# Kernel tuning notes

Hardware: AMD Instinct MI355X
Metric: run time of the kernel (lower is better)

The kernel has to match this reference:

```python
import jax, jax.numpy as jnp
import numpy as np

EPS = 1e-6

def _normalize(v):
    return v / jnp.sqrt(jnp.maximum(jnp.sum(v * v, -1, keepdims=True), EPS))

def _frames(pos):
    # backbone rigid frame from N (atom 0), CA (atom 1), C (atom 2) via Gram-Schmidt
    n, ca, c = pos[..., 0, :], pos[..., 1, :], pos[..., 2, :]
    e1 = _normalize(c - ca)
    v2 = n - ca
    e2 = _normalize(v2 - jnp.sum(e1 * v2, -1, keepdims=True) * e1)
    e3 = jnp.cross(e1, e2)
    R = jnp.stack([e1, e2, e3], axis=-1)  # columns are the local basis
    return R, ca

def _vnorm(d):
    return jnp.sqrt(jnp.maximum(jnp.sum(d * d, -1), EPS))

def setup_inputs():
    L, N, A = 2, 768, 14
    key = jax.random.key(0)
    k1, k2, k3, k4, k5 = jax.random.split(key, 5)
    pred = 3.0 * jax.random.normal(k1, (L, N, A, 3), dtype=jnp.float32)
    gt = 3.0 * jax.random.normal(k2, (N, A, 3), dtype=jnp.float32)
    atom_mask = (jax.random.uniform(k3, (N, A)) > 0.1).astype(jnp.float32)
    batch = jnp.sort(jax.random.randint(k4, (N,), 0, 2)).astype(jnp.int32)
    chain = jnp.sort(jax.random.randint(k5, (N,), 0, 4)).astype(jnp.int32)
    return {"pred": pred, "gt": gt, "atom_mask": atom_mask, "batch": batch, "chain": chain}

def reference(pred, gt, atom_mask, batch, chain):
    L, N, A, _ = pred.shape
    same_item = (batch[:, None] == batch[None, :]).astype(pred.dtype)
    # pair_mask[i, j, a] = mask[i, a] * mask[j, a] * same_item[i, j]
    pair_mask = atom_mask[:, None] * atom_mask[None, :] * same_item[..., None]
    Rp, tp = _frames(pred)   # [L,N,3,3], [L,N,3]
    Rg, tg = _frames(gt)     # [N,3,3],   [N,3]
    # pglobal[l,i,j,a] = Rp[l,i]^T @ (pred[l,j,a] - tp[l,i]) (frame-inverse point application)
    pglobal = (jnp.einsum('lidk,ljad->lijak', Rp, pred)
               - jnp.einsum('lidk,lid->lik', Rp, tp)[:, :, None, None, :])
    gglobal = (jnp.einsum('idk,jad->ijak', Rg, gt)
               - jnp.einsum('idk,id->ik', Rg, tg)[:, None, None, :])
    err = _vnorm(pglobal - gglobal[None])                       # [L,N,N,A]
    fape = jnp.where(pair_mask[None] > 0, err, 0.0).sum(-1)
    fape = fape / jnp.maximum(pair_mask[None].sum(-1), 1e-6)    # [L,N,N]
    rotamer_error = jnp.diagonal(fape, 0, -2, -1)               # [L,N]
    res_mask = (atom_mask > 0).any(-1)
    n_res = jnp.maximum(res_mask.astype(pred.dtype).sum(), 1e-6)
    rotamer_loss = rotamer_error.sum(-1) / n_res                # [L]
    pm2 = (pair_mask > 0).any(-1).astype(pred.dtype)            # [N,N]
    final_ae = fape[-1]
    same_chain = (chain[:, None] == chain[None, :]).astype(pred.dtype) * pm2
    other_chain = (chain[:, None] != chain[None, :]).astype(pred.dtype) * pm2
    # intra/inter coins in the source are zeros_like(bernoulli) == always False -> clip at 10
    clipped = jnp.clip(fape, 0.0, 10.0)
    intra = (clipped * same_chain[None]).sum((-1, -2))
    intra = intra / jnp.maximum(same_chain.sum(), 1e-6) / 10.0
    inter = (clipped * other_chain[None]).sum((-1, -2))
    inter = inter / jnp.maximum(other_chain.sum(), 1e-6) / 10.0
    fape_loss = intra + inter                                   # [L]
    # lDDT on CA atoms (atom index 1) for the last prediction step
    gt_ca = gt[:, 1, :]
    pred_ca = pred[-1, :, 1, :]
    gt_d = _vnorm(gt_ca[:, None] - gt_ca[None, :])
    rm = res_mask.astype(jnp.float32)
    dmask = ((gt_d < 15.0).astype(jnp.float32) * rm[:, None] * rm[None, :]
             * (1.0 - jnp.eye(N, dtype=jnp.float32))).astype(bool)
    d = _vnorm(pred_ca[:, None] - pred_ca[None, :])
    derr = jnp.where(dmask, jnp.abs(gt_d - d), jnp.inf)
    thresholds = jnp.array([0.5, 1.0, 2.0, 4.0], dtype=jnp.float32)
    l = (derr[..., None] < thresholds).astype(jnp.float32).mean(-1)
    lddt_val = jnp.where(dmask, l, 0.0).sum(-1)
    lddt_val = lddt_val / jnp.maximum(dmask.astype(jnp.float32).sum(-1), 1e-6)
    return (fape_loss, rotamer_loss, final_ae, rotamer_error[-1], lddt_val)
```

## Files before the change

### kernel.cpp

```cpp
#include <hip/hip_runtime.h>
#include <math.h>

#define EPS 1e-6f
#define IPB 3

struct F3 { float x, y, z; };
__device__ inline F3 sub3(F3 a, F3 b){return {a.x-b.x,a.y-b.y,a.z-b.z};}
__device__ inline float dot3(F3 a, F3 b){return a.x*b.x+a.y*b.y+a.z*b.z;}
__device__ inline F3 scale3(F3 a,float s){return {a.x*s,a.y*s,a.z*s};}
__device__ inline F3 cross3(F3 a,F3 b){return {a.y*b.z-a.z*b.y, a.z*b.x-a.x*b.z, a.x*b.y-a.y*b.x};}
__device__ inline F3 norm3(F3 v){float s=dot3(v,v);float inv=1.f/sqrtf(fmaxf(s,EPS));return scale3(v,inv);}

__device__ inline void make_frame(const float* __restrict__ base, float R[9], F3& ca) {
    F3 n = {base[0], base[1], base[2]};
    ca   = {base[3], base[4], base[5]};
    F3 c = {base[6], base[7], base[8]};
    F3 e1 = norm3(sub3(c, ca));
    F3 v2 = sub3(n, ca);
    float d = dot3(e1, v2);
    F3 e2 = norm3({v2.x - d*e1.x, v2.y - d*e1.y, v2.z - d*e1.z});
    F3 e3 = cross3(e1, e2);
    R[0]=e1.x; R[1]=e1.y; R[2]=e1.z;
    R[3]=e2.x; R[4]=e2.y; R[5]=e2.z;
    R[6]=e3.x; R[7]=e3.y; R[8]=e3.z;
}

__global__ __launch_bounds__(256) void prep_all_kernel(
    const float* __restrict__ pred, const float* __restrict__ gt,
    const float* __restrict__ atom_mask, const int* __restrict__ batch,
    const int* __restrict__ chain,
    float* __restrict__ Mc, int* __restrict__ packed,
    float* __restrict__ gtca, float* __restrict__ predca,
    float4* __restrict__ predT4, float4* __restrict__ gtT4,
    int L, int N, int A)
{
    int idx = blockIdx.x * blockDim.x + threadIdx.x;

    int totalT = (L + 1) * A * N;
    if (idx < totalT) {
        int z = idx / (A * N);
        int r = idx - z * (A * N);
        int a = r / N;
        int j = r - a * N;
        if (z < L) {
            const float* s = pred + (((size_t)z * N + j) * A + a) * 3;
            predT4[((size_t)z * A + a) * N + j] = make_float4(s[0], s[1], s[2], 0.f);
        } else {
            const float* s = gt + ((size_t)j * A + a) * 3;
            gtT4[(size_t)a * N + j] = make_float4(s[0], s[1], s[2], 0.f);
        }
    }

    if (idx >= L * N) return;
    int l = idx / N, i = idx - l * N;

    float Rg[9]; F3 cag;
    make_frame(gt + (size_t)i * A * 3, Rg, cag);
    float Rp[9]; F3 cap;
    make_frame(pred + ((size_t)l * N + i) * A * 3, Rp, cap);

    float m[9];
    #pragma unroll
    for (int d = 0; d < 3; d++)
        #pragma unroll
        for (int e = 0; e < 3; e++)
            m[d*3+e] = Rp[0*3+d]*Rg[0*3+e] + Rp[1*3+d]*Rg[1*3+e] + Rp[2*3+d]*Rg[2*3+e];
    float c0 = cap.x - (m[0]*cag.x + m[1]*cag.y + m[2]*cag.z);
    float c1 = cap.y - (m[3]*cag.x + m[4]*cag.y + m[5]*cag.z);
    float c2 = cap.z - (m[6]*cag.x + m[7]*cag.y + m[8]*cag.z);

    float* o = Mc + (size_t)idx * 12;
    #pragma unroll
    for (int k = 0; k < 9; k++) o[k] = m[k];
    o[9] = c0; o[10] = c1; o[11] = c2;

    if (l == 0) {
        unsigned mm = 0;
        for (int a = 0; a < A; a++)
            if (atom_mask[(size_t)i * A + a] > 0.f) mm |= (1u << a);
        packed[i] = (int)(mm | ((unsigned)batch[i] << 16) | ((unsigned)chain[i] << 24));
        gtca[i*3] = cag.x; gtca[i*3+1] = cag.y; gtca[i*3+2] = cag.z;
    }
    if (l == L - 1) { predca[i*3] = cap.x; predca[i*3+1] = cap.y; predca[i*3+2] = cap.z; }
}

__global__ __launch_bounds__(256) void fape_kernel(
    const float4* __restrict__ predT4, const float4* __restrict__ gtT4,
    const float* __restrict__ Mc, const int* __restrict__ packed,
    const float* __restrict__ gtca, const float* __restrict__ predca,
    float* __restrict__ part,
    float* __restrict__ out_final, float* __restrict__ out_rot,
    float* __restrict__ out_lddt,
    int L, int N)
{
    int t = threadIdx.x;
    int ib = blockIdx.x, l = blockIdx.y;
    int i0 = ib * IPB;
    bool last = (l == L - 1);

    const float* __restrict__ mcp = Mc + ((size_t)l * N + i0) * 12;
    float M[IPB][12];
    #pragma unroll
    for (int q = 0; q < IPB; q++)
        #pragma unroll
        for (int k = 0; k < 12; k++) M[q][k] = mcp[q*12 + k];

    int mk[IPB], bt[IPB], ch[IPB];
    #pragma unroll
    for (int q = 0; q < IPB; q++) {
        int pk = packed[i0 + q];
        mk[q] = pk & 0xFFFF; bt[q] = (pk >> 16) & 0xFF; ch[q] = (pk >> 24) & 0xFF;
    }

    float gx[IPB],gy[IPB],gz[IPB],px[IPB],py[IPB],pz[IPB];
    #pragma unroll
    for (int q = 0; q < IPB; q++) { gx[q]=gy[q]=gz[q]=px[q]=py[q]=pz[q]=0.f; }
    if (last) {
        #pragma unroll
        for (int q = 0; q < IPB; q++) {
            int i = i0 + q;
            gx[q]=gtca[i*3]; gy[q]=gtca[i*3+1]; gz[q]=gtca[i*3+2];
            px[q]=predca[i*3]; py[q]=predca[i*3+1]; pz[q]=predca[i*3+2];
        }
    }

    const float4* __restrict__ xT4 = predT4 + (size_t)l * 14 * N;

    float a_ss=0.f, a_so=0.f, a_cs=0.f, a_co=0.f, a_rot=0.f;
    float ls[IPB], lc[IPB];
    #pragma unroll
    for (int q = 0; q < IPB; q++) { ls[q]=0.f; lc[q]=0.f; }

    for (int j = t; j < N; j += 256) {
        int pkj = packed[j];
        int mskj = pkj & 0xFFFF;
        int bj = (pkj >> 16) & 0xFF, cj = (pkj >> 24) & 0xFF;

        int mj[IPB]; bool pm[IPB]; bool anyp = false;
        #pragma unroll
        for (int q = 0; q < IPB; q++) {
            mj[q] = mk[q] & mskj;
            pm[q] = (bj == bt[q]) && (mj[q] != 0);
            anyp = anyp || pm[q];
        }
        float num[IPB];
        #pragma unroll
        for (int q = 0; q < IPB; q++) num[q] = 0.f;

        if (__any((int)anyp)) {
            #pragma unroll
            for (int a = 0; a < 14; a++) {
                float4 Y = gtT4[(size_t)a * N + j];
                float4 X = xT4[(size_t)a * N + j];
                #pragma unroll
                for (int q = 0; q < IPB; q++) {
                    float d0 = X.x - (M[q][0]*Y.x + M[q][1]*Y.y + M[q][2]*Y.z + M[q][9]);
                    float d1 = X.y - (M[q][3]*Y.x + M[q][4]*Y.y + M[q][5]*Y.z + M[q][10]);
                    float d2 = X.z - (M[q][6]*Y.x + M[q][7]*Y.y + M[q][8]*Y.z + M[q][11]);
                    num[q] += (float)((mj[q] >> a) & 1) * sqrtf(fmaxf(d0*d0+d1*d1+d2*d2, EPS));
                }
            }
        }

        #pragma unroll
        for (int q = 0; q < IPB; q++) {
            float fv = pm[q] ? num[q] / (float)__popc((unsigned)mj[q]) : 0.f;
            int i = i0 + q;
            if (last) {
                out_final[(size_t)i * N + j] = fv;
                if (j == i) out_rot[i] = fv;
            }
            if (j == i) a_rot += fv;
            if (pm[q]) {
                float cl = fminf(fv, 10.f);
                if (ch[q] == cj) { a_ss += cl; a_cs += 1.f; } else { a_so += cl; a_co += 1.f; }
            }
        }

        if (last) {
            float4 CG = gtT4[(size_t)N + j];
            float4 CP = xT4[(size_t)N + j];
            #pragma unroll
            for (int q = 0; q < IPB; q++) {
                if ((mk[q] != 0) && (mskj != 0) && (j != i0 + q)) {
                    float dx=gx[q]-CG.x, dy=gy[q]-CG.y, dz=gz[q]-CG.z;
                    float gd = sqrtf(fmaxf(dx*dx+dy*dy+dz*dz, EPS));
                    if (gd < 15.f) {
                        float ex=px[q]-CP.x, ey=py[q]-CP.y, ez=pz[q]-CP.z;
                        float pd = sqrtf(fmaxf(ex*ex+ey*ey+ez*ez, EPS));
                        float de = fabsf(gd - pd);
                        ls[q] += ((de<0.5f?1.f:0.f)+(de<1.f?1.f:0.f)+(de<2.f?1.f:0.f)+(de<4.f?1.f:0.f))*0.25f;
                        lc[q] += 1.f;
                    }
                }
            }
        }
    }

    float vals[11];
    vals[0]=a_ss; vals[1]=a_so; vals[2]=a_cs; vals[3]=a_co; vals[4]=a_rot;
    #pragma unroll
    for (int q = 0; q < IPB; q++) { vals[5+q]=ls[q]; vals[5+IPB+q]=lc[q]; }
    #pragma unroll
    for (int k = 0; k < 11; k++)
        for (int o = 32; o > 0; o >>= 1) vals[k] += __shfl_down(vals[k], o, 64);

    __shared__ float red[4][11];
    int wave = t >> 6, lane = t & 63;
    if (lane == 0) {
        #pragma unroll
        for (int k = 0; k < 11; k++) red[wave][k] = vals[k];
    }
    __syncthreads();
    if (t == 0) {
        float v[11];
        #pragma unroll
        for (int k = 0; k < 11; k++)
            v[k] = red[0][k] + red[1][k] + red[2][k] + red[3][k];
        float* p = part + ((size_t)l * (N / IPB) + ib) * 8;
        p[0]=v[0]; p[1]=v[1]; p[2]=v[2]; p[3]=v[3]; p[4]=v[4];
        if (last) {
            #pragma unroll
            for (int q = 0; q < IPB; q++)
                out_lddt[i0 + q] = v[5+q] / fmaxf(v[5+IPB+q], 1e-6f);
        }
    }
}

__global__ __launch_bounds__(256) void reduce_kernel(
    const int* __restrict__ packed, const float* __restrict__ part,
    float* __restrict__ out, int L, int N)
{
    int t = threadIdx.x;
    int BPL = N / IPB;
    float ss[4]={0,0,0,0}, so[4]={0,0,0,0}, rt[4]={0,0,0,0};
    float cs=0.f, co=0.f;
    for (int b = t; b < BPL * L; b += 256) {
        int l = b / BPL;
        const float* p = part + (size_t)b * 8;
        ss[l] += p[0]; so[l] += p[1]; rt[l] += p[4];
        if (l == 0) { cs += p[2]; co += p[3]; }
    }
    float nr = 0.f;
    for (int i = t; i < N; i += 256)
        nr += ((packed[i] & 0xFFFF) != 0) ? 1.f : 0.f;

    __shared__ float red[4];
    int wave = t >> 6, lane = t & 63;
    float vals[11];
    vals[0]=cs; vals[1]=co; vals[2]=nr;
    for (int l = 0; l < L; l++) { vals[3+l]=ss[l]; vals[3+L+l]=so[l]; vals[3+2*L+l]=rt[l]; }
    float res[11];
    for (int k = 0; k < 3 + 3*L; k++) {
        float v = vals[k];
        for (int o = 32; o > 0; o >>= 1) v += __shfl_down(v, o, 64);
        __syncthreads();
        if (lane == 0) red[wave] = v;
        __syncthreads();
        res[k] = red[0] + red[1] + red[2] + red[3];
    }
    if (t == 0) {
        float csf = fmaxf(res[0], 1e-6f);
        float cof = fmaxf(res[1], 1e-6f);
        float nrm = fmaxf(res[2], 1e-6f);
        for (int l = 0; l < L; l++) {
            out[l]     = res[3+l] / csf / 10.f + res[3+L+l] / cof / 10.f;
            out[L + l] = res[3+2*L+l] / nrm;
        }
    }
}

extern "C" void kernel_launch(void* const* d_in, const int* in_sizes, int n_in,
                              void* d_out, int out_size, void* d_ws, size_t ws_size,
                              hipStream_t stream)
{
    const float* pred      = (const float*)d_in[0];
    const float* gt        = (const float*)d_in[1];
    const float* atom_mask = (const float*)d_in[2];
    const int*   batch     = (const int*)d_in[3];
    const int*   chain     = (const int*)d_in[4];

    int N = in_sizes[3];
    int A = in_sizes[2] / N;
    int L = in_sizes[0] / (N * A * 3);

    float* out = (float*)d_out;
    float* out_final = out + 2 * L;
    float* out_rot   = out_final + (size_t)N * N;
    float* out_lddt  = out_rot + N;

    float* ws = (float*)d_ws;
    float4* predT4 = (float4*)ws;
    float4* gtT4   = predT4 + (size_t)L * A * N;
    float*  Mc     = (float*)(gtT4 + (size_t)A * N);
    float*  gtca   = Mc + (size_t)L * N * 12;
    float*  predca = gtca + (size_t)N * 3;
    float*  part   = predca + (size_t)N * 3;
    int*    packed = (int*)(part + (size_t)L * (N / IPB) * 8);

    int totalT = (L + 1) * A * N;
    prep_all_kernel<<<(totalT + 255) / 256, 256, 0, stream>>>(
        pred, gt, atom_mask, batch, chain,
        Mc, packed, gtca, predca, predT4, gtT4, L, N, A);

    dim3 grid(N / IPB, L);
    fape_kernel<<<grid, 256, 0, stream>>>(
        predT4, gtT4, Mc, packed, gtca, predca, part,
        out_final, out_rot, out_lddt, L, N);

    reduce_kernel<<<1, 256, 0, stream>>>(packed, part, out, L, N);
}
```

Measured before the change: 96.68 us.

## Split FAPE j-range across blocks and shrink rows per block

The FAPE kernel's j loop is split into three slices across extra grid blocks, and rows per block drop from 3 to 2. This raises the block count so the many CUs get more parallel work, with each thread handling one j. Per-slice partials, including the lDDT sums, are written to a larger partial buffer. The final lDDT division moves into the single-block reduce kernel. The cost is more redundant per-block frame loads and more reduction work done serially in one block.

```diff
diff --git a/kernel.cpp b/kernel.cpp
--- a/kernel.cpp
+++ b/kernel.cpp
@@ -2,7 +2,8 @@
 #include <math.h>
 
 #define EPS 1e-6f
-#define IPB 3
+#define IPB 2
+#define JS  3
 
 struct F3 { float x, y, z; };
 __device__ inline F3 sub3(F3 a, F3 b){return {a.x-b.x,a.y-b.y,a.z-b.z};}
@@ -90,12 +91,14 @@
     const float* __restrict__ gtca, const float* __restrict__ predca,
     float* __restrict__ part,
     float* __restrict__ out_final, float* __restrict__ out_rot,
-    float* __restrict__ out_lddt,
     int L, int N)
 {
     int t = threadIdx.x;
-    int ib = blockIdx.x, l = blockIdx.y;
+    int ib = blockIdx.x;
+    int l  = blockIdx.y / JS;
+    int s  = blockIdx.y - l * JS;
     int i0 = ib * IPB;
+    int jlo = s * (N / JS), jhi = jlo + (N / JS);
     bool last = (l == L - 1);
 
     const float* __restrict__ mcp = Mc + ((size_t)l * N + i0) * 12;
@@ -131,7 +134,7 @@
     #pragma unroll
     for (int q = 0; q < IPB; q++) { ls[q]=0.f; lc[q]=0.f; }
 
-    for (int j = t; j < N; j += 256) {
+    for (int j = jlo + t; j < jhi; j += 256) {
         int pkj = packed[j];
         int mskj = pkj & 0xFFFF;
         int bj = (pkj >> 16) & 0xFF, cj = (pkj >> 24) & 0xFF;
@@ -197,60 +200,68 @@
         }
     }
 
-    float vals[11];
+    float vals[9];
     vals[0]=a_ss; vals[1]=a_so; vals[2]=a_cs; vals[3]=a_co; vals[4]=a_rot;
     #pragma unroll
     for (int q = 0; q < IPB; q++) { vals[5+q]=ls[q]; vals[5+IPB+q]=lc[q]; }
     #pragma unroll
-    for (int k = 0; k < 11; k++)
+    for (int k = 0; k < 9; k++)
         for (int o = 32; o > 0; o >>= 1) vals[k] += __shfl_down(vals[k], o, 64);
 
-    __shared__ float red[4][11];
+    __shared__ float red[4][9];
     int wave = t >> 6, lane = t & 63;
     if (lane == 0) {
         #pragma unroll
-        for (int k = 0; k < 11; k++) red[wave][k] = vals[k];
+        for (int k = 0; k < 9; k++) red[wave][k] = vals[k];
     }
     __syncthreads();
     if (t == 0) {
-        float v[11];
-        #pragma unroll
-        for (int k = 0; k < 11; k++)
-            v[k] = red[0][k] + red[1][k] + red[2][k] + red[3][k];
-        float* p = part + ((size_t)l * (N / IPB) + ib) * 8;
-        p[0]=v[0]; p[1]=v[1]; p[2]=v[2]; p[3]=v[3]; p[4]=v[4];
-        if (last) {
-            #pragma unroll
-            for (int q = 0; q < IPB; q++)
-                out_lddt[i0 + q] = v[5+q] / fmaxf(v[5+IPB+q], 1e-6f);
-        }
+        float* p = part + ((size_t)blockIdx.y * (N / IPB) + ib) * 12;
+        #pragma unroll
+        for (int k = 0; k < 9; k++)
+            p[k] = red[0][k] + red[1][k] + red[2][k] + red[3][k];
     }
 }
 
 __global__ __launch_bounds__(256) void reduce_kernel(
     const int* __restrict__ packed, const float* __restrict__ part,
-    float* __restrict__ out, int L, int N)
+    float* __restrict__ out, float* __restrict__ out_lddt, int L, int N)
 {
     int t = threadIdx.x;
     int BPL = N / IPB;
+    int ROWS = L * JS;
+
     float ss[4]={0,0,0,0}, so[4]={0,0,0,0}, rt[4]={0,0,0,0};
     float cs=0.f, co=0.f;
-    for (int b = t; b < BPL * L; b += 256) {
-        int l = b / BPL;
-        const float* p = part + (size_t)b * 8;
+    for (int b = t; b < ROWS * BPL; b += 256) {
+        int row = b / BPL;
+        int l = row / JS;
+        const float* p = part + (size_t)b * 12;
         ss[l] += p[0]; so[l] += p[1]; rt[l] += p[4];
         if (l == 0) { cs += p[2]; co += p[3]; }
     }
+
+    for (int i = t; i < N; i += 256) {
+        int ib = i / IPB, q = i - ib * IPB;
+        float lsum = 0.f, lcnt = 0.f;
+        for (int s = 0; s < JS; s++) {
+            const float* p = part + (((size_t)((L - 1) * JS + s)) * BPL + ib) * 12;
+            lsum += p[5 + q];
+            lcnt += p[5 + IPB + q];
+        }
+        out_lddt[i] = lsum / fmaxf(lcnt, 1e-6f);
+    }
+
     float nr = 0.f;
     for (int i = t; i < N; i += 256)
         nr += ((packed[i] & 0xFFFF) != 0) ? 1.f : 0.f;
 
     __shared__ float red[4];
     int wave = t >> 6, lane = t & 63;
-    float vals[11];
+    float vals[15];
     vals[0]=cs; vals[1]=co; vals[2]=nr;
     for (int l = 0; l < L; l++) { vals[3+l]=ss[l]; vals[3+L+l]=so[l]; vals[3+2*L+l]=rt[l]; }
-    float res[11];
+    float res[15];
     for (int k = 0; k < 3 + 3*L; k++) {
         float v = vals[k];
         for (int o = 32; o > 0; o >>= 1) v += __shfl_down(v, o, 64);
@@ -296,17 +307,17 @@
     float*  gtca   = Mc + (size_t)L * N * 12;
     float*  predca = gtca + (size_t)N * 3;
     float*  part   = predca + (size_t)N * 3;
-    int*    packed = (int*)(part + (size_t)L * (N / IPB) * 8);
+    int*    packed = (int*)(part + (size_t)L * JS * (N / IPB) * 12);
 
     int totalT = (L + 1) * A * N;
     prep_all_kernel<<<(totalT + 255) / 256, 256, 0, stream>>>(
         pred, gt, atom_mask, batch, chain,
         Mc, packed, gtca, predca, predT4, gtT4, L, N, A);
 
-    dim3 grid(N / IPB, L);
+    dim3 grid(N / IPB, L * JS);
     fape_kernel<<<grid, 256, 0, stream>>>(
         predT4, gtT4, Mc, packed, gtca, predca, part,
-        out_final, out_rot, out_lddt, L, N);
-
-    reduce_kernel<<<1, 256, 0, stream>>>(packed, part, out, L, N);
-}
+        out_final, out_rot, L, N);
+
+    reduce_kernel<<<1, 256, 0, stream>>>(packed, part, out, out_lddt, L, N);
+}
```

Result: faster. 93.11 us (-3.7%).

## Fuse prep into FAPE kernel, read raw AoS inputs, and use two residues per block

Applied to the files above, without the earlier changes.

Removes the separate prep kernel that transposed coordinates into float4 SoA buffers and precomputed frames. Each FAPE block now builds its own frame-composition matrices and atom-mask bits directly from the raw inputs, and reads per-j coordinates as contiguous 42-float rows into registers. IPB drops from 3 to 2, so there are more blocks. This saves one launch and the workspace round trip. In exchange, every block recomputes the mask bits for all j, and the strided AoS loads coalesce worse than the old SoA float4 loads.

```diff
diff --git a/kernel.cpp b/kernel.cpp
--- a/kernel.cpp
+++ b/kernel.cpp
@@ -2,7 +2,9 @@
 #include <math.h>
 
 #define EPS 1e-6f
-#define IPB 3
+#define IPB 2
+#define NA 14
+#define ROW 42
 
 struct F3 { float x, y, z; };
 __device__ inline F3 sub3(F3 a, F3 b){return {a.x-b.x,a.y-b.y,a.z-b.z};}
@@ -25,69 +27,10 @@
     R[6]=e3.x; R[7]=e3.y; R[8]=e3.z;
 }
 
-__global__ __launch_bounds__(256) void prep_all_kernel(
+__global__ __launch_bounds__(256) void fape_kernel(
     const float* __restrict__ pred, const float* __restrict__ gt,
     const float* __restrict__ atom_mask, const int* __restrict__ batch,
     const int* __restrict__ chain,
-    float* __restrict__ Mc, int* __restrict__ packed,
-    float* __restrict__ gtca, float* __restrict__ predca,
-    float4* __restrict__ predT4, float4* __restrict__ gtT4,
-    int L, int N, int A)
-{
-    int idx = blockIdx.x * blockDim.x + threadIdx.x;
-
-    int totalT = (L + 1) * A * N;
-    if (idx < totalT) {
-        int z = idx / (A * N);
-        int r = idx - z * (A * N);
-        int a = r / N;
-        int j = r - a * N;
-        if (z < L) {
-            const float* s = pred + (((size_t)z * N + j) * A + a) * 3;
-            predT4[((size_t)z * A + a) * N + j] = make_float4(s[0], s[1], s[2], 0.f);
-        } else {
-            const float* s = gt + ((size_t)j * A + a) * 3;
-            gtT4[(size_t)a * N + j] = make_float4(s[0], s[1], s[2], 0.f);
-        }
-    }
-
-    if (idx >= L * N) return;
-    int l = idx / N, i = idx - l * N;
-
-    float Rg[9]; F3 cag;
-    make_frame(gt + (size_t)i * A * 3, Rg, cag);
-    float Rp[9]; F3 cap;
-    make_frame(pred + ((size_t)l * N + i) * A * 3, Rp, cap);
-
-    float m[9];
-    #pragma unroll
-    for (int d = 0; d < 3; d++)
-        #pragma unroll
-        for (int e = 0; e < 3; e++)
-            m[d*3+e] = Rp[0*3+d]*Rg[0*3+e] + Rp[1*3+d]*Rg[1*3+e] + Rp[2*3+d]*Rg[2*3+e];
-    float c0 = cap.x - (m[0]*cag.x + m[1]*cag.y + m[2]*cag.z);
-    float c1 = cap.y - (m[3]*cag.x + m[4]*cag.y + m[5]*cag.z);
-    float c2 = cap.z - (m[6]*cag.x + m[7]*cag.y + m[8]*cag.z);
-
-    float* o = Mc + (size_t)idx * 12;
-    #pragma unroll
-    for (int k = 0; k < 9; k++) o[k] = m[k];
-    o[9] = c0; o[10] = c1; o[11] = c2;
-
-    if (l == 0) {
-        unsigned mm = 0;
-        for (int a = 0; a < A; a++)
-            if (atom_mask[(size_t)i * A + a] > 0.f) mm |= (1u << a);
-        packed[i] = (int)(mm | ((unsigned)batch[i] << 16) | ((unsigned)chain[i] << 24));
-        gtca[i*3] = cag.x; gtca[i*3+1] = cag.y; gtca[i*3+2] = cag.z;
-    }
-    if (l == L - 1) { predca[i*3] = cap.x; predca[i*3+1] = cap.y; predca[i*3+2] = cap.z; }
-}
-
-__global__ __launch_bounds__(256) void fape_kernel(
-    const float4* __restrict__ predT4, const float4* __restrict__ gtT4,
-    const float* __restrict__ Mc, const int* __restrict__ packed,
-    const float* __restrict__ gtca, const float* __restrict__ predca,
     float* __restrict__ part,
     float* __restrict__ out_final, float* __restrict__ out_rot,
     float* __restrict__ out_lddt,
@@ -98,33 +41,36 @@
     int i0 = ib * IPB;
     bool last = (l == L - 1);
 
-    const float* __restrict__ mcp = Mc + ((size_t)l * N + i0) * 12;
     float M[IPB][12];
-    #pragma unroll
-    for (int q = 0; q < IPB; q++)
-        #pragma unroll
-        for (int k = 0; k < 12; k++) M[q][k] = mcp[q*12 + k];
-
     int mk[IPB], bt[IPB], ch[IPB];
+    float gx[IPB],gy[IPB],gz[IPB],px[IPB],py[IPB],pz[IPB];
     #pragma unroll
     for (int q = 0; q < IPB; q++) {
-        int pk = packed[i0 + q];
-        mk[q] = pk & 0xFFFF; bt[q] = (pk >> 16) & 0xFF; ch[q] = (pk >> 24) & 0xFF;
-    }
-
-    float gx[IPB],gy[IPB],gz[IPB],px[IPB],py[IPB],pz[IPB];
-    #pragma unroll
-    for (int q = 0; q < IPB; q++) { gx[q]=gy[q]=gz[q]=px[q]=py[q]=pz[q]=0.f; }
-    if (last) {
-        #pragma unroll
-        for (int q = 0; q < IPB; q++) {
-            int i = i0 + q;
-            gx[q]=gtca[i*3]; gy[q]=gtca[i*3+1]; gz[q]=gtca[i*3+2];
-            px[q]=predca[i*3]; py[q]=predca[i*3+1]; pz[q]=predca[i*3+2];
-        }
-    }
-
-    const float4* __restrict__ xT4 = predT4 + (size_t)l * 14 * N;
+        int i = i0 + q;
+        float Rg[9]; F3 cag;
+        make_frame(gt + (size_t)i * ROW, Rg, cag);
+        float Rp[9]; F3 cap;
+        make_frame(pred + ((size_t)l * N + i) * ROW, Rp, cap);
+        #pragma unroll
+        for (int d = 0; d < 3; d++)
+            #pragma unroll
+            for (int e = 0; e < 3; e++)
+                M[q][d*3+e] = Rp[0*3+d]*Rg[0*3+e] + Rp[1*3+d]*Rg[1*3+e] + Rp[2*3+d]*Rg[2*3+e];
+        M[q][9]  = cap.x - (M[q][0]*cag.x + M[q][1]*cag.y + M[q][2]*cag.z);
+        M[q][10] = cap.y - (M[q][3]*cag.x + M[q][4]*cag.y + M[q][5]*cag.z);
+        M[q][11] = cap.z - (M[q][6]*cag.x + M[q][7]*cag.y + M[q][8]*cag.z);
+
+        unsigned mm = 0;
+        const float* am = atom_mask + (size_t)i * NA;
+        #pragma unroll
+        for (int a = 0; a < NA; a++) mm |= (am[a] > 0.f) ? (1u << a) : 0u;
+        mk[q] = (int)mm; bt[q] = batch[i]; ch[q] = chain[i];
+
+        gx[q]=cag.x; gy[q]=cag.y; gz[q]=cag.z;
+        px[q]=cap.x; py[q]=cap.y; pz[q]=cap.z;
+    }
+
+    const float* __restrict__ Xbase = pred + (size_t)l * N * ROW;
 
     float a_ss=0.f, a_so=0.f, a_cs=0.f, a_co=0.f, a_rot=0.f;
     float ls[IPB], lc[IPB];
@@ -132,14 +78,19 @@
     for (int q = 0; q < IPB; q++) { ls[q]=0.f; lc[q]=0.f; }
 
     for (int j = t; j < N; j += 256) {
-        int pkj = packed[j];
-        int mskj = pkj & 0xFFFF;
-        int bj = (pkj >> 16) & 0xFF, cj = (pkj >> 24) & 0xFF;
+        unsigned mskj = 0;
+        const float* amj = atom_mask + (size_t)j * NA;
+        #pragma unroll
+        for (int a = 0; a < NA; a++) mskj |= (amj[a] > 0.f) ? (1u << a) : 0u;
+        int bj = batch[j], cj = chain[j];
+
+        const float* __restrict__ Yp = gt + (size_t)j * ROW;
+        const float* __restrict__ Xp = Xbase + (size_t)j * ROW;
 
         int mj[IPB]; bool pm[IPB]; bool anyp = false;
         #pragma unroll
         for (int q = 0; q < IPB; q++) {
-            mj[q] = mk[q] & mskj;
+            mj[q] = mk[q] & (int)mskj;
             pm[q] = (bj == bt[q]) && (mj[q] != 0);
             anyp = anyp || pm[q];
         }
@@ -149,15 +100,22 @@
 
         if (__any((int)anyp)) {
             #pragma unroll
-            for (int a = 0; a < 14; a++) {
-                float4 Y = gtT4[(size_t)a * N + j];
-                float4 X = xT4[(size_t)a * N + j];
+            for (int ah = 0; ah < 2; ah++) {
+                float xr[21], yr[21];
                 #pragma unroll
-                for (int q = 0; q < IPB; q++) {
-                    float d0 = X.x - (M[q][0]*Y.x + M[q][1]*Y.y + M[q][2]*Y.z + M[q][9]);
-                    float d1 = X.y - (M[q][3]*Y.x + M[q][4]*Y.y + M[q][5]*Y.z + M[q][10]);
-                    float d2 = X.z - (M[q][6]*Y.x + M[q][7]*Y.y + M[q][8]*Y.z + M[q][11]);
-                    num[q] += (float)((mj[q] >> a) & 1) * sqrtf(fmaxf(d0*d0+d1*d1+d2*d2, EPS));
+                for (int k = 0; k < 21; k++) { xr[k] = Xp[ah*21 + k]; yr[k] = Yp[ah*21 + k]; }
+                #pragma unroll
+                for (int a = 0; a < 7; a++) {
+                    int aa = ah*7 + a;
+                    float Yx = yr[a*3], Yy = yr[a*3+1], Yz = yr[a*3+2];
+                    float Xx = xr[a*3], Xy = xr[a*3+1], Xz = xr[a*3+2];
+                    #pragma unroll
+                    for (int q = 0; q < IPB; q++) {
+                        float d0 = Xx - (M[q][0]*Yx + M[q][1]*Yy + M[q][2]*Yz + M[q][9]);
+                        float d1 = Xy - (M[q][3]*Yx + M[q][4]*Yy + M[q][5]*Yz + M[q][10]);
+                        float d2 = Xz - (M[q][6]*Yx + M[q][7]*Yy + M[q][8]*Yz + M[q][11]);
+                        num[q] += (float)((mj[q] >> aa) & 1) * sqrtf(fmaxf(d0*d0+d1*d1+d2*d2, EPS));
+                    }
                 }
             }
         }
@@ -178,15 +136,15 @@
         }
 
         if (last) {
-            float4 CG = gtT4[(size_t)N + j];
-            float4 CP = xT4[(size_t)N + j];
+            float CGx = Yp[3], CGy = Yp[4], CGz = Yp[5];
+            float CPx = Xp[3], CPy = Xp[4], CPz = Xp[5];
             #pragma unroll
             for (int q = 0; q < IPB; q++) {
                 if ((mk[q] != 0) && (mskj != 0) && (j != i0 + q)) {
-                    float dx=gx[q]-CG.x, dy=gy[q]-CG.y, dz=gz[q]-CG.z;
+                    float dx=gx[q]-CGx, dy=gy[q]-CGy, dz=gz[q]-CGz;
                     float gd = sqrtf(fmaxf(dx*dx+dy*dy+dz*dz, EPS));
                     if (gd < 15.f) {
-                        float ex=px[q]-CP.x, ey=py[q]-CP.y, ez=pz[q]-CP.z;
+                        float ex=px[q]-CPx, ey=py[q]-CPy, ez=pz[q]-CPz;
                         float pd = sqrtf(fmaxf(ex*ex+ey*ey+ez*ez, EPS));
                         float de = fabsf(gd - pd);
                         ls[q] += ((de<0.5f?1.f:0.f)+(de<1.f?1.f:0.f)+(de<2.f?1.f:0.f)+(de<4.f?1.f:0.f))*0.25f;
@@ -197,25 +155,25 @@
         }
     }
 
-    float vals[11];
+    float vals[9];
     vals[0]=a_ss; vals[1]=a_so; vals[2]=a_cs; vals[3]=a_co; vals[4]=a_rot;
     #pragma unroll
     for (int q = 0; q < IPB; q++) { vals[5+q]=ls[q]; vals[5+IPB+q]=lc[q]; }
     #pragma unroll
-    for (int k = 0; k < 11; k++)
+    for (int k = 0; k < 9; k++)
         for (int o = 32; o > 0; o >>= 1) vals[k] += __shfl_down(vals[k], o, 64);
 
-    __shared__ float red[4][11];
+    __shared__ float red[4][9];
     int wave = t >> 6, lane = t & 63;
     if (lane == 0) {
         #pragma unroll
-        for (int k = 0; k < 11; k++) red[wave][k] = vals[k];
+        for (int k = 0; k < 9; k++) red[wave][k] = vals[k];
     }
     __syncthreads();
     if (t == 0) {
-        float v[11];
-        #pragma unroll
-        for (int k = 0; k < 11; k++)
+        float v[9];
+        #pragma unroll
+        for (int k = 0; k < 9; k++)
             v[k] = red[0][k] + red[1][k] + red[2][k] + red[3][k];
         float* p = part + ((size_t)l * (N / IPB) + ib) * 8;
         p[0]=v[0]; p[1]=v[1]; p[2]=v[2]; p[3]=v[3]; p[4]=v[4];
@@ -228,7 +186,7 @@
 }
 
 __global__ __launch_bounds__(256) void reduce_kernel(
-    const int* __restrict__ packed, const float* __restrict__ part,
+    const float* __restrict__ atom_mask, const float* __restrict__ part,
     float* __restrict__ out, int L, int N)
 {
     int t = threadIdx.x;
@@ -242,15 +200,20 @@
         if (l == 0) { cs += p[2]; co += p[3]; }
     }
     float nr = 0.f;
-    for (int i = t; i < N; i += 256)
-        nr += ((packed[i] & 0xFFFF) != 0) ? 1.f : 0.f;
+    for (int i = t; i < N; i += 256) {
+        const float* am = atom_mask + (size_t)i * NA;
+        bool any = false;
+        #pragma unroll
+        for (int a = 0; a < NA; a++) any = any || (am[a] > 0.f);
+        nr += any ? 1.f : 0.f;
+    }
 
     __shared__ float red[4];
     int wave = t >> 6, lane = t & 63;
-    float vals[11];
+    float vals[15];
     vals[0]=cs; vals[1]=co; vals[2]=nr;
     for (int l = 0; l < L; l++) { vals[3+l]=ss[l]; vals[3+L+l]=so[l]; vals[3+2*L+l]=rt[l]; }
-    float res[11];
+    float res[15];
     for (int k = 0; k < 3 + 3*L; k++) {
         float v = vals[k];
         for (int o = 32; o > 0; o >>= 1) v += __shfl_down(v, o, 64);
@@ -283,30 +246,19 @@
     int N = in_sizes[3];
     int A = in_sizes[2] / N;
     int L = in_sizes[0] / (N * A * 3);
+    (void)A;
 
     float* out = (float*)d_out;
     float* out_final = out + 2 * L;
     float* out_rot   = out_final + (size_t)N * N;
     float* out_lddt  = out_rot + N;
 
-    float* ws = (float*)d_ws;
-    float4* predT4 = (float4*)ws;
-    float4* gtT4   = predT4 + (size_t)L * A * N;
-    float*  Mc     = (float*)(gtT4 + (size_t)A * N);
-    float*  gtca   = Mc + (size_t)L * N * 12;
-    float*  predca = gtca + (size_t)N * 3;
-    float*  part   = predca + (size_t)N * 3;
-    int*    packed = (int*)(part + (size_t)L * (N / IPB) * 8);
-
-    int totalT = (L + 1) * A * N;
-    prep_all_kernel<<<(totalT + 255) / 256, 256, 0, stream>>>(
-        pred, gt, atom_mask, batch, chain,
-        Mc, packed, gtca, predca, predT4, gtT4, L, N, A);
+    float* part = (float*)d_ws;
 
     dim3 grid(N / IPB, L);
     fape_kernel<<<grid, 256, 0, stream>>>(
-        predT4, gtT4, Mc, packed, gtca, predca, part,
+        pred, gt, atom_mask, batch, chain, part,
         out_final, out_rot, out_lddt, L, N);
 
-    reduce_kernel<<<1, 256, 0, stream>>>(packed, part, out, L, N);
-}
+    reduce_kernel<<<1, 256, 0, stream>>>(atom_mask, part, out, L, N);
+}
```

New measurement: 98.04 us. No clear change (+1.4%).
